# Performance work log

Measured on AMD Instinct MI355X. Metric: run time of the kernel, lower is better.

## Reference

```python
import jax, jax.numpy as jnp
import numpy as np

B, S, D, H = 32, 1024, 256, 8
HD = D // H  # 32, remainder 0 so all heads have equal dim
EPS = 1e-5


def layer_norm(x, gamma, beta):
    mu = jnp.mean(x, axis=-1, keepdims=True)
    var = jnp.mean(jnp.square(x - mu), axis=-1, keepdims=True)
    return (x - mu) * jax.lax.rsqrt(var + EPS) * gamma + beta


def setup_inputs() -> dict:
    key = jax.random.key(0)
    ks = jax.random.split(key, 8)
    sc = 1.0 / np.sqrt(D)
    return {
        "x": jax.random.normal(ks[0], (B, S, D), jnp.float32),
        "wq": jax.random.normal(ks[1], (D, D), jnp.float32) * sc,
        "wk": jax.random.normal(ks[2], (D, D), jnp.float32) * sc,
        "wv": jax.random.normal(ks[3], (D, D), jnp.float32) * sc,
        "g1": jnp.ones((D,), jnp.float32),
        "beta1": jnp.zeros((D,), jnp.float32),
        "g2": jnp.ones((D,), jnp.float32),
        "beta2": jnp.zeros((D,), jnp.float32),
        "w_f1": jax.random.normal(ks[4], (D, D), jnp.float32) * sc,
        "b_f1": jnp.zeros((D,), jnp.float32),
        "w_f2": jax.random.normal(ks[5], (D, D), jnp.float32) * sc,
        "b_f2": jnp.zeros((D,), jnp.float32),
    }


def reference(x, wq, wk, wv, g1, beta1, g2, beta2, w_f1, b_f1, w_f2, b_f2):
    xn = layer_norm(x, g1, beta1)
    # QKV projections (no bias)
    q = (xn @ wq).reshape(B, S, H, HD)
    k = (xn @ wk).reshape(B, S, H, HD)
    v = (xn @ wv).reshape(B, S, H, HD)
    # NOTE: original applies NO 1/sqrt(d) scaling
    scores = jnp.einsum("bqhd,bkhd->bhqk", q, k)
    attn = jax.nn.softmax(scores, axis=-1)
    ctx = jnp.einsum("bhqk,bkhd->bqhd", attn, v).reshape(B, S, D)
    # residual + norm2
    a = layer_norm(ctx + x, g2, beta2)
    # FFN: Dense(D, relu) -> Dense(D)  (dropout inactive at inference)
    ffn = jax.nn.relu(a @ w_f1 + b_f1) @ w_f2 + b_f2
    return a + ffn
```

## Files before the change

### kernel.cpp

```cpp
#include <hip/hip_runtime.h>
#include <stdint.h>

typedef unsigned short ushort_t;
typedef __attribute__((ext_vector_type(8))) short short8;
typedef __attribute__((ext_vector_type(4))) float f32x4;
typedef __attribute__((ext_vector_type(4))) unsigned short ushort4v;

#define NBATCH 32
#define SEQ 1024
#define DIM 256
#define NH 8
#define ROWS (NBATCH * SEQ)

__device__ __forceinline__ ushort_t f2bf(float f) {
    uint32_t u = __float_as_uint(f);
    u += 0x7fffu + ((u >> 16) & 1u);
    return (ushort_t)(u >> 16);
}
__device__ __forceinline__ float bf2f(ushort_t h) {
    return __uint_as_float(((uint32_t)h) << 16);
}
__device__ __forceinline__ float exp2_fast(float x) {
    float r;
    asm("v_exp_f32 %0, %1" : "=v"(r) : "v"(x));
    return r;
}

typedef __attribute__((address_space(3))) void lds_void_t;
typedef const __attribute__((address_space(1))) void glob_void_t;
__device__ __forceinline__ void gld_lds16(const void* g, void* l) {
    __builtin_amdgcn_global_load_lds((glob_void_t*)g, (lds_void_t*)l, 16, 0, 0);
}

__global__ __launch_bounds__(256) void ln1_prep(
    const float* __restrict__ x, const float* __restrict__ g,
    const float* __restrict__ beta, const float* __restrict__ wq,
    const float* __restrict__ wk, const float* __restrict__ wv,
    const float* __restrict__ wf1, const float* __restrict__ wf2,
    ushort_t* __restrict__ xn, ushort_t* __restrict__ wqkvT,
    ushort_t* __restrict__ wf1T, ushort_t* __restrict__ wf2T) {
    int blk = blockIdx.x;
    if (blk < 8192) {
        int wid = threadIdx.x >> 6, lane = threadIdx.x & 63;
        size_t row = (size_t)blk * 4 + wid;
        size_t base = row * 256 + lane * 4;
        float4 v = *(const float4*)(x + base);
        float s = v.x + v.y + v.z + v.w;
        float s2 = v.x * v.x + v.y * v.y + v.z * v.z + v.w * v.w;
#pragma unroll
        for (int msk = 1; msk < 64; msk <<= 1) {
            s += __shfl_xor(s, msk);
            s2 += __shfl_xor(s2, msk);
        }
        float mu = s * (1.f / 256.f);
        float var = s2 * (1.f / 256.f) - mu * mu;
        float rs = rsqrtf(var + 1e-5f);
        const float4 gv = *(const float4*)(g + lane * 4);
        const float4 bv = *(const float4*)(beta + lane * 4);
        ushort4v o;
        o[0] = f2bf((v.x - mu) * rs * gv.x + bv.x);
        o[1] = f2bf((v.y - mu) * rs * gv.y + bv.y);
        o[2] = f2bf((v.z - mu) * rs * gv.z + bv.z);
        o[3] = f2bf((v.w - mu) * rs * gv.w + bv.w);
        *(ushort4v*)(xn + base) = o;
    } else {
        int n = blk - 8192;
        int k = threadIdx.x;
        if (n < 768) {
            const float* w = (n < 256) ? wq : (n < 512 ? wk : wv);
            int nn = n & 255;
            float v = w[k * 256 + nn];
            if (n < 256) v *= 1.4426950408889634f;
            wqkvT[n * 256 + k] = f2bf(v);
        } else if (n < 1024) {
            int nn = n - 768;
            wf1T[nn * 256 + k] = f2bf(wf1[k * 256 + nn]);
        } else {
            int nn = n - 1024;
            wf2T[nn * 256 + k] = f2bf(wf2[k * 256 + nn]);
        }
    }
}

__global__ __launch_bounds__(256) void ln2_kernel(
    const float* __restrict__ x, const ushort_t* __restrict__ ctx,
    const float* __restrict__ g, const float* __restrict__ beta,
    ushort_t* __restrict__ out) {
    int wid = threadIdx.x >> 6, lane = threadIdx.x & 63;
    size_t row = (size_t)blockIdx.x * 4 + wid;
    size_t base = row * 256 + lane * 4;
    float4 v = *(const float4*)(x + base);
    ushort4v c = *(const ushort4v*)(ctx + base);
    v.x += bf2f(c[0]); v.y += bf2f(c[1]);
    v.z += bf2f(c[2]); v.w += bf2f(c[3]);
    float s  = v.x + v.y + v.z + v.w;
    float s2 = v.x * v.x + v.y * v.y + v.z * v.z + v.w * v.w;
#pragma unroll
    for (int msk = 1; msk < 64; msk <<= 1) {
        s  += __shfl_xor(s, msk);
        s2 += __shfl_xor(s2, msk);
    }
    float mu  = s * (1.f / 256.f);
    float var = s2 * (1.f / 256.f) - mu * mu;
    float rs  = rsqrtf(var + 1e-5f);
    const float4 gv = *(const float4*)(g + lane * 4);
    const float4 bv = *(const float4*)(beta + lane * 4);
    ushort4v o;
    o[0] = f2bf((v.x - mu) * rs * gv.x + bv.x);
    o[1] = f2bf((v.y - mu) * rs * gv.y + bv.y);
    o[2] = f2bf((v.z - mu) * rs * gv.z + bv.z);
    o[3] = f2bf((v.w - mu) * rs * gv.w + bv.w);
    *(ushort4v*)(out + base) = o;
}

template <int EPI>
__global__ __launch_bounds__(256) void gemm_bt(
    const ushort_t* __restrict__ A, const ushort_t* __restrict__ B,
    void* __restrict__ Cp, const float* __restrict__ bias,
    const ushort_t* __restrict__ res, ushort_t* __restrict__ kout,
    ushort_t* __restrict__ vout, int nbn, int ldc) {
    __shared__ ushort_t lds_a[8192];
    __shared__ ushort_t lds_b[8192];
    int cpx = gridDim.x >> 3;
    int blk = (blockIdx.x & 7) * cpx + (blockIdx.x >> 3);
    int bn = blk % nbn, bm = blk / nbn;
    int m0 = bm * 128, n0 = bn * 128;
    int tid = threadIdx.x, wid = tid >> 6, lane = tid & 63;
    int fr = lane & 15, g = lane >> 4;
    int wm = (wid >> 1) * 64, wn = (wid & 1) * 64;

    f32x4 acc[4][4];
    const f32x4 fz = {0.f, 0.f, 0.f, 0.f};
#pragma unroll
    for (int m = 0; m < 4; m++)
#pragma unroll
        for (int n = 0; n < 4; n++) acc[m][n] = fz;

    for (int kt = 0; kt < 256; kt += 64) {
#pragma unroll
        for (int i = 0; i < 4; i++) {
            const ushort_t* as =
                A + (size_t)(m0 + i * 32 + (tid >> 3)) * 256 + kt + (tid & 7) * 8;
            gld_lds16(as, &lds_a[i * 2048 + wid * 512]);
            const ushort_t* bs =
                B + (size_t)(n0 + i * 32 + (tid >> 3)) * 256 + kt + (tid & 7) * 8;
            gld_lds16(bs, &lds_b[i * 2048 + wid * 512]);
        }
        __syncthreads();
#pragma unroll
        for (int s = 0; s < 2; s++) {
            short8 af[4], bfr[4];
#pragma unroll
            for (int m = 0; m < 4; m++)
                af[m] =
                    *(const short8*)&lds_a[(wm + m * 16 + fr) * 64 + s * 32 + g * 8];
#pragma unroll
            for (int n = 0; n < 4; n++)
                bfr[n] =
                    *(const short8*)&lds_b[(wn + n * 16 + fr) * 64 + s * 32 + g * 8];
#pragma unroll
            for (int m = 0; m < 4; m++)
#pragma unroll
                for (int n = 0; n < 4; n++)
                    acc[m][n] = __builtin_amdgcn_mfma_f32_16x16x32_bf16(
                        af[m], bfr[n], acc[m][n], 0, 0, 0);
        }
        __syncthreads();
    }

#pragma unroll
    for (int m = 0; m < 4; m++)
#pragma unroll
        for (int n = 0; n < 4; n++) {
            int col = n0 + wn + n * 16 + fr;
            int rowbase = m0 + wm + m * 16 + g * 4;
            if (EPI == 3 && col >= 512) {
                int hh = (col >> 5) & 7, hd = col & 31;
                int nn = hd >> 4, frv = hd & 15;
                int bb = rowbase >> 10;
                int key = rowbase & 1023;
                int slot0 = (key & ~31) + (((key & 15) >> 2) << 3) +
                            (((key >> 4) & 1) << 2);
                int t64 = slot0 >> 6, kk = (slot0 & 63) >> 5;
                int gv = (slot0 & 31) >> 3, e0 = slot0 & 7;
                ushort4v o;
                o[0] = f2bf(acc[m][n][0]);
                o[1] = f2bf(acc[m][n][1]);
                o[2] = f2bf(acc[m][n][2]);
                o[3] = f2bf(acc[m][n][3]);
                *(ushort4v*)(vout + (size_t)(bb * 8 + hh) * 32768 + t64 * 2048 +
                             (kk * 2 + nn) * 512 + (gv * 16 + frv) * 8 + e0) = o;
            } else if (EPI == 3 && col >= 256) {
                int hh = (col >> 5) & 7, hd = col & 31;
                int gk = hd >> 3, e = hd & 7;
                int bb = rowbase >> 10;
                int s = rowbase & 1023;
                size_t base = (size_t)(bb * 8 + hh) * 32768 + (s >> 4) * 512 +
                              gk * 128 + e;
#pragma unroll
                for (int j = 0; j < 4; j++)
                    kout[base + ((s & 15) + j) * 8] = f2bf(acc[m][n][j]);
            } else {
                float bv = (EPI == 1 || EPI == 2) ? bias[col] : 0.f;
#pragma unroll
                for (int j = 0; j < 4; j++) {
                    size_t row = (size_t)(rowbase + j);
                    float v = acc[m][n][j] + bv;
                    if (EPI == 1) v = fmaxf(v, 0.f);
                    if (EPI == 2) {
                        v += bf2f(res[row * 256 + col]);
                        ((float*)Cp)[row * ldc + col] = v;
                    } else {
                        ((ushort_t*)Cp)[row * ldc + col] = f2bf(v);
                    }
                }
            }
        }
}

__global__ __launch_bounds__(256, 4) void attn_kernel(
    const ushort_t* __restrict__ q, const ushort_t* __restrict__ kpk,
    const ushort_t* __restrict__ vpk, ushort_t* __restrict__ ctx) {
    int cpx = gridDim.x >> 3;
    int wgid = (blockIdx.x & 7) * cpx + (blockIdx.x >> 3);
    int bh = wgid >> 3, qt = wgid & 7;
    int b = bh >> 3, h = bh & 7;
    int tid = threadIdx.x, wid = tid >> 6, lane = tid & 63;
    int fr = lane & 15, g = lane >> 4;
    int q0 = qt * 128 + wid * 32;
    const ushort_t* qbase = q + (size_t)b * SEQ * 256;
    const ushort_t* kpb = kpk + (size_t)bh * 32768;
    const ushort_t* vpb = vpk + (size_t)bh * 32768;
    const int l8 = lane * 8;

    short8 qb[2];
#pragma unroll
    for (int m = 0; m < 2; m++)
        qb[m] = *(const short8*)(qbase + (size_t)(q0 + m * 16 + fr) * 256 +
                                 h * 32 + g * 8);

    f32x4 acc[2][2], asum[2];
    const f32x4 fz = {0.f, 0.f, 0.f, 0.f};
#pragma unroll
    for (int m = 0; m < 2; m++) {
        acc[m][0] = fz;
        acc[m][1] = fz;
        asum[m] = fz;
    }
    short8 ones8;
#pragma unroll
    for (int i = 0; i < 8; i++) ones8[i] = (short)0x3f80;

    short8 kreg[4];
#pragma unroll
    for (int n = 0; n < 4; n++)
        kreg[n] = *(const short8*)(kpb + n * 512 + l8);

    for (int kv = 0; kv < SEQ; kv += 64) {
        short8 vreg[2][2];
#pragma unroll
        for (int kk = 0; kk < 2; kk++) {
            vreg[kk][0] =
                *(const short8*)(vpb + (kv >> 6) * 2048 + (kk * 2) * 512 + l8);
            vreg[kk][1] = *(const short8*)(vpb + (kv >> 6) * 2048 +
                                           (kk * 2 + 1) * 512 + l8);
        }

        f32x4 s[4][2];
#pragma unroll
        for (int n = 0; n < 4; n++)
#pragma unroll
            for (int m = 0; m < 2; m++)
                s[n][m] = __builtin_amdgcn_mfma_f32_16x16x32_bf16(kreg[n], qb[m],
                                                                  fz, 0, 0, 0);

        if (kv + 64 < SEQ) {
#pragma unroll
            for (int n = 0; n < 4; n++)
                kreg[n] = *(const short8*)(kpb + ((kv + 64) >> 4) * 512 +
                                           n * 512 + l8);
        }

#pragma unroll
        for (int kk = 0; kk < 2; kk++) {
#pragma unroll
            for (int m = 0; m < 2; m++) {
                float p0 = exp2_fast(s[2 * kk][m][0]);
                float p1 = exp2_fast(s[2 * kk][m][1]);
                float p2 = exp2_fast(s[2 * kk][m][2]);
                float p3 = exp2_fast(s[2 * kk][m][3]);
                float p4 = exp2_fast(s[2 * kk + 1][m][0]);
                float p5 = exp2_fast(s[2 * kk + 1][m][1]);
                float p6 = exp2_fast(s[2 * kk + 1][m][2]);
                float p7 = exp2_fast(s[2 * kk + 1][m][3]);
                union { short8 s8; uint32_t u[4]; } pa;
                asm("v_cvt_pk_bf16_f32 %0, %1, %2"
                    : "=v"(pa.u[0]) : "v"(p0), "v"(p1));
                asm("v_cvt_pk_bf16_f32 %0, %1, %2"
                    : "=v"(pa.u[1]) : "v"(p2), "v"(p3));
                asm("v_cvt_pk_bf16_f32 %0, %1, %2"
                    : "=v"(pa.u[2]) : "v"(p4), "v"(p5));
                asm("v_cvt_pk_bf16_f32 %0, %1, %2"
                    : "=v"(pa.u[3]) : "v"(p6), "v"(p7));
                acc[m][0] = __builtin_amdgcn_mfma_f32_16x16x32_bf16(
                    pa.s8, vreg[kk][0], acc[m][0], 0, 0, 0);
                acc[m][1] = __builtin_amdgcn_mfma_f32_16x16x32_bf16(
                    pa.s8, vreg[kk][1], acc[m][1], 0, 0, 0);
                asum[m] = __builtin_amdgcn_mfma_f32_16x16x32_bf16(
                    pa.s8, ones8, asum[m], 0, 0, 0);
            }
        }
    }

#pragma unroll
    for (int m = 0; m < 2; m++)
#pragma unroll
        for (int j = 0; j < 4; j++) {
            float inv = 1.f / asum[m][j];
#pragma unroll
            for (int n = 0; n < 2; n++) {
                size_t row = (size_t)b * SEQ + q0 + m * 16 + g * 4 + j;
                ctx[row * 256 + h * 32 + n * 16 + fr] =
                    f2bf(acc[m][n][j] * inv);
            }
        }
}

extern "C" void kernel_launch(void* const* d_in, const int* in_sizes, int n_in,
                              void* d_out, int out_size, void* d_ws,
                              size_t ws_size, hipStream_t stream) {
    const float* x   = (const float*)d_in[0];
    const float* wq  = (const float*)d_in[1];
    const float* wk  = (const float*)d_in[2];
    const float* wv  = (const float*)d_in[3];
    const float* g1  = (const float*)d_in[4];
    const float* be1 = (const float*)d_in[5];
    const float* g2  = (const float*)d_in[6];
    const float* be2 = (const float*)d_in[7];
    const float* wf1 = (const float*)d_in[8];
    const float* bf1 = (const float*)d_in[9];
    const float* wf2 = (const float*)d_in[10];
    const float* bf2 = (const float*)d_in[11];

    char* ws = (char*)d_ws;
    const size_t SZ16M = (size_t)ROWS * 256 * 2;
    ushort_t* wqkvT = (ushort_t*)(ws);
    ushort_t* wf1T  = (ushort_t*)(ws + 393216);
    ushort_t* wf2T  = (ushort_t*)(ws + 524288);
    ushort_t* xn    = (ushort_t*)(ws + 655360);
    ushort_t* qonly = (ushort_t*)(ws + 655360 + SZ16M);
    ushort_t* kpk   = (ushort_t*)(ws + 655360 + 2 * SZ16M);
    ushort_t* vpk   = (ushort_t*)(ws + 655360 + 3 * SZ16M);
    ushort_t* ctxb  = (ushort_t*)(ws + 655360 + 4 * SZ16M);
    ushort_t* ab    = (ushort_t*)(ws + 655360 + 5 * SZ16M);
    ushort_t* hb    = xn;

    ln1_prep<<<dim3(9472), dim3(256), 0, stream>>>(
        x, g1, be1, wq, wk, wv, wf1, wf2, xn, wqkvT, wf1T, wf2T);
    gemm_bt<3><<<dim3(256 * 6), dim3(256), 0, stream>>>(
        xn, wqkvT, (void*)qonly, nullptr, nullptr, kpk, vpk, 6, 256);
    attn_kernel<<<dim3(2048), dim3(256), 0, stream>>>(qonly, kpk, vpk, ctxb);
    ln2_kernel<<<dim3(ROWS / 4), dim3(256), 0, stream>>>(x, ctxb, g2, be2, ab);
    gemm_bt<1><<<dim3(256 * 2), dim3(256), 0, stream>>>(
        ab, wf1T, (void*)hb, bf1, nullptr, nullptr, nullptr, 2, 256);
    gemm_bt<2><<<dim3(256 * 2), dim3(256), 0, stream>>>(
        hb, wf2T, d_out, bf2, ab, nullptr, nullptr, 2, 256);
}
```

Before: 129.4 us.

## Fuse FFN two GEMMs into one kernel keeping hidden activations in LDS

```diff
diff --git a/kernel.cpp b/kernel.cpp
--- a/kernel.cpp
+++ b/kernel.cpp
@@ -119,8 +119,8 @@
     void* __restrict__ Cp, const float* __restrict__ bias,
     const ushort_t* __restrict__ res, ushort_t* __restrict__ kout,
     ushort_t* __restrict__ vout, int nbn, int ldc) {
-    __shared__ ushort_t lds_a[8192];
-    __shared__ ushort_t lds_b[8192];
+    __shared__ ushort_t lds_a[4096];
+    __shared__ ushort_t lds_b[4096];
     int cpx = gridDim.x >> 3;
     int blk = (blockIdx.x & 7) * cpx + (blockIdx.x >> 3);
     int bn = blk % nbn, bm = blk / nbn;
@@ -136,35 +136,30 @@
 #pragma unroll
         for (int n = 0; n < 4; n++) acc[m][n] = fz;
 
-    for (int kt = 0; kt < 256; kt += 64) {
-#pragma unroll
-        for (int i = 0; i < 4; i++) {
+    for (int kt = 0; kt < 256; kt += 32) {
+#pragma unroll
+        for (int i = 0; i < 2; i++) {
             const ushort_t* as =
-                A + (size_t)(m0 + i * 32 + (tid >> 3)) * 256 + kt + (tid & 7) * 8;
+                A + (size_t)(m0 + i * 64 + (tid >> 2)) * 256 + kt + (tid & 3) * 8;
             gld_lds16(as, &lds_a[i * 2048 + wid * 512]);
             const ushort_t* bs =
-                B + (size_t)(n0 + i * 32 + (tid >> 3)) * 256 + kt + (tid & 7) * 8;
+                B + (size_t)(n0 + i * 64 + (tid >> 2)) * 256 + kt + (tid & 3) * 8;
             gld_lds16(bs, &lds_b[i * 2048 + wid * 512]);
         }
         __syncthreads();
-#pragma unroll
-        for (int s = 0; s < 2; s++) {
-            short8 af[4], bfr[4];
-#pragma unroll
-            for (int m = 0; m < 4; m++)
-                af[m] =
-                    *(const short8*)&lds_a[(wm + m * 16 + fr) * 64 + s * 32 + g * 8];
+        short8 af[4], bfr[4];
+#pragma unroll
+        for (int m = 0; m < 4; m++)
+            af[m] = *(const short8*)&lds_a[(wm + m * 16 + fr) * 32 + g * 8];
+#pragma unroll
+        for (int n = 0; n < 4; n++)
+            bfr[n] = *(const short8*)&lds_b[(wn + n * 16 + fr) * 32 + g * 8];
+#pragma unroll
+        for (int m = 0; m < 4; m++)
 #pragma unroll
             for (int n = 0; n < 4; n++)
-                bfr[n] =
-                    *(const short8*)&lds_b[(wn + n * 16 + fr) * 64 + s * 32 + g * 8];
-#pragma unroll
-            for (int m = 0; m < 4; m++)
-#pragma unroll
-                for (int n = 0; n < 4; n++)
-                    acc[m][n] = __builtin_amdgcn_mfma_f32_16x16x32_bf16(
-                        af[m], bfr[n], acc[m][n], 0, 0, 0);
-        }
+                acc[m][n] = __builtin_amdgcn_mfma_f32_16x16x32_bf16(
+                    af[m], bfr[n], acc[m][n], 0, 0, 0);
         __syncthreads();
     }
 
@@ -218,6 +213,101 @@
         }
 }
 
+__global__ __launch_bounds__(256) void ffn_fused(
+    const ushort_t* __restrict__ A, const ushort_t* __restrict__ W1,
+    const ushort_t* __restrict__ W2, const float* __restrict__ b1,
+    const float* __restrict__ b2, float* __restrict__ out) {
+    __shared__ ushort_t a_lds[64 * 32];
+    __shared__ ushort_t w_lds[256 * 32];
+    __shared__ ushort_t h_lds[64 * 264];
+    int m0 = blockIdx.x * 64;
+    int tid = threadIdx.x, wid = tid >> 6, lane = tid & 63;
+    int fr = lane & 15, g = lane >> 4;
+    int wn = wid * 64;
+
+    f32x4 acc[4][4];
+    const f32x4 fz = {0.f, 0.f, 0.f, 0.f};
+#pragma unroll
+    for (int m = 0; m < 4; m++)
+#pragma unroll
+        for (int n = 0; n < 4; n++) acc[m][n] = fz;
+
+    for (int kt = 0; kt < 256; kt += 32) {
+        gld_lds16(A + (size_t)(m0 + (tid >> 2)) * 256 + kt + (tid & 3) * 8,
+                  &a_lds[wid * 512]);
+#pragma unroll
+        for (int i = 0; i < 4; i++)
+            gld_lds16(W1 + (size_t)(i * 64 + (tid >> 2)) * 256 + kt +
+                          (tid & 3) * 8,
+                      &w_lds[i * 2048 + wid * 512]);
+        __syncthreads();
+        short8 af[4], bfr[4];
+#pragma unroll
+        for (int m = 0; m < 4; m++)
+            af[m] = *(const short8*)&a_lds[(m * 16 + fr) * 32 + g * 8];
+#pragma unroll
+        for (int n = 0; n < 4; n++)
+            bfr[n] = *(const short8*)&w_lds[(wn + n * 16 + fr) * 32 + g * 8];
+#pragma unroll
+        for (int m = 0; m < 4; m++)
+#pragma unroll
+            for (int n = 0; n < 4; n++)
+                acc[m][n] = __builtin_amdgcn_mfma_f32_16x16x32_bf16(
+                    af[m], bfr[n], acc[m][n], 0, 0, 0);
+        __syncthreads();
+    }
+#pragma unroll
+    for (int m = 0; m < 4; m++)
+#pragma unroll
+        for (int n = 0; n < 4; n++) {
+            int col = wn + n * 16 + fr;
+            float bv = b1[col];
+#pragma unroll
+            for (int j = 0; j < 4; j++) {
+                int row = m * 16 + g * 4 + j;
+                h_lds[row * 264 + col] = f2bf(fmaxf(acc[m][n][j] + bv, 0.f));
+            }
+            acc[m][n] = fz;
+        }
+    __syncthreads();
+
+    for (int kt = 0; kt < 256; kt += 32) {
+#pragma unroll
+        for (int i = 0; i < 4; i++)
+            gld_lds16(W2 + (size_t)(i * 64 + (tid >> 2)) * 256 + kt +
+                          (tid & 3) * 8,
+                      &w_lds[i * 2048 + wid * 512]);
+        __syncthreads();
+        short8 af[4], bfr[4];
+#pragma unroll
+        for (int m = 0; m < 4; m++)
+            af[m] = *(const short8*)&h_lds[(m * 16 + fr) * 264 + kt + g * 8];
+#pragma unroll
+        for (int n = 0; n < 4; n++)
+            bfr[n] = *(const short8*)&w_lds[(wn + n * 16 + fr) * 32 + g * 8];
+#pragma unroll
+        for (int m = 0; m < 4; m++)
+#pragma unroll
+            for (int n = 0; n < 4; n++)
+                acc[m][n] = __builtin_amdgcn_mfma_f32_16x16x32_bf16(
+                    af[m], bfr[n], acc[m][n], 0, 0, 0);
+        __syncthreads();
+    }
+#pragma unroll
+    for (int m = 0; m < 4; m++)
+#pragma unroll
+        for (int n = 0; n < 4; n++) {
+            int col = wn + n * 16 + fr;
+            float bv = b2[col];
+#pragma unroll
+            for (int j = 0; j < 4; j++) {
+                size_t row = (size_t)(m0 + m * 16 + g * 4 + j);
+                out[row * 256 + col] =
+                    acc[m][n][j] + bv + bf2f(A[row * 256 + col]);
+            }
+        }
+}
+
 __global__ __launch_bounds__(256, 4) void attn_kernel(
     const ushort_t* __restrict__ q, const ushort_t* __restrict__ kpk,
     const ushort_t* __restrict__ vpk, ushort_t* __restrict__ ctx) {
@@ -353,7 +443,6 @@
     ushort_t* vpk   = (ushort_t*)(ws + 655360 + 3 * SZ16M);
     ushort_t* ctxb  = (ushort_t*)(ws + 655360 + 4 * SZ16M);
     ushort_t* ab    = (ushort_t*)(ws + 655360 + 5 * SZ16M);
-    ushort_t* hb    = xn;
 
     ln1_prep<<<dim3(9472), dim3(256), 0, stream>>>(
         x, g1, be1, wq, wk, wv, wf1, wf2, xn, wqkvT, wf1T, wf2T);
@@ -361,8 +450,6 @@
         xn, wqkvT, (void*)qonly, nullptr, nullptr, kpk, vpk, 6, 256);
     attn_kernel<<<dim3(2048), dim3(256), 0, stream>>>(qonly, kpk, vpk, ctxb);
     ln2_kernel<<<dim3(ROWS / 4), dim3(256), 0, stream>>>(x, ctxb, g2, be2, ab);
-    gemm_bt<1><<<dim3(256 * 2), dim3(256), 0, stream>>>(
-        ab, wf1T, (void*)hb, bf1, nullptr, nullptr, nullptr, 2, 256);
-    gemm_bt<2><<<dim3(256 * 2), dim3(256), 0, stream>>>(
-        hb, wf2T, d_out, bf2, ab, nullptr, nullptr, 2, 256);
-}
+    ffn_fused<<<dim3(512), dim3(256), 0, stream>>>(ab, wf1T, wf2T, bf1, bf2,
+                                                   (float*)d_out);
+}
```

After: 118.2 us, median of 3. 1.1x faster.
